# Kernel tuning notes

Hardware: AMD Instinct MI355X
Metric: run time of the kernel (lower is better)

Reference implementation:

```python
import jax, jax.numpy as jnp
import numpy as np

B, S, H, NH = 2, 2048, 2048, 16
HD = H // NH


def setup_inputs() -> dict:
    key = jax.random.key(0)
    ks = jax.random.split(key, 10)
    s = 1.0 / np.sqrt(H)
    x = jax.random.normal(ks[0], (B, S, H), dtype=jnp.float32)
    # additive causal mask: 0 on/below diagonal, -1e9 above
    causal = jnp.tril(jnp.ones((S, S), dtype=bool))
    mask = jnp.where(causal, 0.0, -1e9).astype(jnp.float32)[None, None]
    return {
        "x": x,
        "mask": mask,
        "wq": jax.random.normal(ks[1], (H, H), jnp.float32) * s,
        "bq": jnp.zeros((H,), jnp.float32),
        "wk": jax.random.normal(ks[2], (H, H), jnp.float32) * s,
        "bk": jnp.zeros((H,), jnp.float32),
        "wv": jax.random.normal(ks[3], (H, H), jnp.float32) * s,
        "bv": jnp.zeros((H,), jnp.float32),
        "wo": jax.random.normal(ks[4], (H, H), jnp.float32) * s,
        "bo": jnp.zeros((H,), jnp.float32),
    }


def reference(x, mask, wq, bq, wk, bk, wv, bv, wo, bo):
    b, s, _ = x.shape
    scale = HD ** (-0.5)
    # projections -> [b, nh, s, hd]
    def split_heads(t):
        return t.reshape(b, s, NH, HD).transpose(0, 2, 1, 3)
    q = split_heads(x @ wq + bq)
    k = split_heads(x @ wk + bk)
    v = split_heads(x @ wv + bv)
    scores = jnp.einsum('bhqd,bhkd->bhqk', q, k) * scale + mask
    attn = jax.nn.softmax(scores, axis=-1)
    out = jnp.einsum('bhqk,bhkd->bhqd', attn, v)
    out = out.transpose(0, 2, 1, 3).reshape(b, s, H)
    return out @ wo + bo
```

## Files before the change

### kernel.cpp

```cpp
#include <hip/hip_runtime.h>


using bf16x8 = __attribute__((ext_vector_type(8))) short;
using bf16x4 = __attribute__((ext_vector_type(4))) short;
using f32x4  = __attribute__((ext_vector_type(4))) float;

#define S_LEN 2048
#define NHEAD 16
#define HDIM  128
#define HID   2048

__device__ __forceinline__ unsigned short f2bf(float f) {
    unsigned int u = __float_as_uint(f);
    u += 0x7fffu + ((u >> 16) & 1u);
    return (unsigned short)(u >> 16);
}
__device__ __forceinline__ void gl2lds16(const void* g, void* l) {
    __builtin_amdgcn_global_load_lds(
        (const __attribute__((address_space(1))) void*)g,
        (__attribute__((address_space(3))) void*)l, 16, 0, 0);
}

__device__ __forceinline__ f32x4 pv_mfma(bf16x4 a, bf16x4 b, f32x4 c) {
#if defined(__HIP_DEVICE_COMPILE__)
#if __has_builtin(__builtin_amdgcn_mfma_f32_16x16x16bf16_1k)
    return __builtin_amdgcn_mfma_f32_16x16x16bf16_1k(a, b, c, 0, 0, 0);
#else
    asm("v_mfma_f32_16x16x16_bf16 %0, %1, %2, %0" : "+v"(c) : "v"(a), "v"(b));
    return c;
#endif
#else
    (void)a; (void)b;
    return c;
#endif
}

__global__ void convert_x(const float* __restrict__ x, unsigned short* __restrict__ xb) {
    int i = (blockIdx.x * 256 + threadIdx.x) * 4;
    float4 v = *(const float4*)(x + i);
    ushort4 o;
    o.x = f2bf(v.x); o.y = f2bf(v.y); o.z = f2bf(v.z); o.w = f2bf(v.w);
    *(ushort4*)(xb + i) = o;
}

__global__ void convert_wt(const float* __restrict__ w0, const float* __restrict__ w1,
                           const float* __restrict__ w2, const float* __restrict__ w3,
                           unsigned short* __restrict__ t0, unsigned short* __restrict__ t1,
                           unsigned short* __restrict__ t2, unsigned short* __restrict__ t3) {
    __shared__ float tile[64][65];
    int z = blockIdx.z;
    const float* src = (z == 0) ? w0 : (z == 1) ? w1 : (z == 2) ? w2 : w3;
    unsigned short* dst = (z == 0) ? t0 : (z == 1) ? t1 : (z == 2) ? t2 : t3;
    int r0 = blockIdx.y * 64, c0 = blockIdx.x * 64;
    int t = threadIdx.x;
    for (int i = t; i < 64 * 64; i += 256) {
        int r = i >> 6, c = i & 63;
        tile[r][c] = src[(size_t)(r0 + r) * HID + c0 + c];
    }
    __syncthreads();
    for (int i = t; i < 64 * 64; i += 256) {
        int r = i & 63, c = i >> 6;
        dst[(size_t)(c0 + c) * HID + r0 + r] = f2bf(tile[r][c]);
    }
}

__device__ __forceinline__ void ldfrag(bf16x8* av, bf16x8* bv,
                                       const unsigned short* AD, const unsigned short* BD,
                                       int arow, int brow, int sw) {
    av[0] = *(const bf16x8*)(AD + arow + sw);
    av[1] = *(const bf16x8*)(AD + arow + 1024 + sw);
    av[2] = *(const bf16x8*)(AD + arow + 2048 + sw);
    av[3] = *(const bf16x8*)(AD + arow + 3072 + sw);
    bv[0] = *(const bf16x8*)(BD + brow + sw);
    bv[1] = *(const bf16x8*)(BD + brow + 1024 + sw);
    bv[2] = *(const bf16x8*)(BD + brow + 2048 + sw);
    bv[3] = *(const bf16x8*)(BD + brow + 3072 + sw);
}

__device__ __forceinline__ void mfma16(const bf16x8* av, const bf16x8* bv, f32x4 (&acc)[4][4]) {
#pragma unroll
    for (int mi = 0; mi < 4; ++mi)
#pragma unroll
        for (int jj = 0; jj < 4; ++jj)
            acc[mi][jj] = __builtin_amdgcn_mfma_f32_16x16x32_bf16(av[mi], bv[jj], acc[mi][jj], 0, 0, 0);
}

template <int MODE>
__launch_bounds__(512, 2)
__global__ void gemm8(const unsigned short* __restrict__ A,
                      const unsigned short* __restrict__ Bt0,
                      const unsigned short* __restrict__ Bt1,
                      const unsigned short* __restrict__ Bt2,
                      const float* __restrict__ bias0,
                      const float* __restrict__ bias1,
                      const float* __restrict__ bias2,
                      unsigned short* __restrict__ C0,
                      unsigned short* __restrict__ C1,
                      unsigned short* __restrict__ C2,
                      float* __restrict__ Cf) {
    __shared__ __align__(16) unsigned short lds[49152];
    unsigned short* const A0 = lds;
    unsigned short* const A1 = lds + 8192;
    unsigned short* const B0 = lds + 16384;
    unsigned short* const B1 = lds + 32768;

    const int CPX = (MODE == 1) ? 96 : 32;
    int vb = (blockIdx.x & 7) * CPX + (blockIdx.x >> 3);
    int m0  = (vb & 31) * 128;
    int n0g = (vb >> 5) * 256;

    const unsigned short* Bt = Bt0;
    const float* bias = bias0;
    unsigned short* C = C0;
    int z = 0;
    if (MODE == 1) {
        z = n0g >> 11;
        if (z == 1) { Bt = Bt1; bias = bias1; C = C1; }
        else if (z == 2) { Bt = Bt2; bias = bias2; C = C2; }
    }
    int nb0 = n0g & 2047;

    int tid = threadIdx.x;
    int lane = tid & 63;
    int wv_ = tid >> 6;
    int wr = wv_ >> 2, wc = wv_ & 3;
    int l15 = lane & 15, quad = lane >> 4;

    int tr = tid >> 3;
    int tc = ((tid & 7) ^ (tr & 7)) << 3;
    const unsigned short* gA = A  + (size_t)(m0  + tr) * HID + tc;
    const unsigned short* gB = Bt + (size_t)(nb0 + tr) * HID + tc;
    const int td8 = tid * 8;

    int arow = (wr * 64 + l15) * 64;
    int brow = (wc * 64 + l15) * 64;
    int sw0 = ((quad ^ (l15 & 7)) << 3);
    int sw1 = (((4 + quad) ^ (l15 & 7)) << 3);

    f32x4 acc[4][4];
#pragma unroll
    for (int i = 0; i < 4; ++i)
#pragma unroll
        for (int j = 0; j < 4; ++j) acc[i][j] = (f32x4){0.f, 0.f, 0.f, 0.f};

    bf16x8 avA[4], bvA[4], avB[4], bvB[4];

#define STAGE8(kt, AD, BD) do { int _kc = (kt) * 64;                        \
    gl2lds16(gA + _kc,              (AD) + td8);                            \
    gl2lds16(gA + 64 * HID + _kc,   (AD) + 4096 + td8);                     \
    gl2lds16(gB + _kc,              (BD) + td8);                            \
    gl2lds16(gB + 64 * HID + _kc,   (BD) + 4096 + td8);                     \
    gl2lds16(gB + 128 * HID + _kc,  (BD) + 8192 + td8);                     \
    gl2lds16(gB + 192 * HID + _kc,  (BD) + 12288 + td8); } while (0)

#define SCHED0() __builtin_amdgcn_sched_barrier(0)
#define BAR()   do { asm volatile("" ::: "memory");                                \
                     __builtin_amdgcn_s_barrier();                                 \
                     asm volatile("" ::: "memory"); } while (0)
#define W_LGKM8() do { asm volatile("s_waitcnt lgkmcnt(8)" ::: "memory"); SCHED0(); } while (0)
#define W_LGKM0() do { asm volatile("s_waitcnt lgkmcnt(0)" ::: "memory"); SCHED0(); } while (0)
#define W_VM6()   do { asm volatile("s_waitcnt vmcnt(6)" ::: "memory");   SCHED0(); } while (0)

#define ITER(AD, BD, AN, BN_, ks) do {                                             \
    ldfrag(avB, bvB, AD, BD, arow, brow, sw1);      \
    W_LGKM8();                                                \
    __builtin_amdgcn_s_setprio(1);                                                 \
    mfma16(avA, bvA, acc);                                 \
    __builtin_amdgcn_s_setprio(0);                                                 \
    W_LGKM0();                                      \
    BAR();                                                                         \
    STAGE8(ks, AD, BD);                                \
    W_VM6();                                               \
    BAR();                                                                         \
    ldfrag(avA, bvA, AN, BN_, arow, brow, sw0);   \
    SCHED0();                                                                      \
    __builtin_amdgcn_s_setprio(1);                                                 \
    mfma16(avB, bvB, acc);                            \
    __builtin_amdgcn_s_setprio(0);                                                 \
} while (0)

    STAGE8(0, A0, B0);
    STAGE8(1, A1, B1);
    W_VM6();
    BAR();
    ldfrag(avA, bvA, A0, B0, arow, brow, sw0);

    for (int t = 0; t < 30; t += 2) {
        ITER(A0, B0, A1, B1, t + 2);
        ITER(A1, B1, A0, B0, t + 3);
    }
    ITER(A0, B0, A1, B1, 31);
    ldfrag(avB, bvB, A1, B1, arow, brow, sw1);
    W_LGKM8();
    __builtin_amdgcn_s_setprio(1);
    mfma16(avA, bvA, acc);
    __builtin_amdgcn_s_setprio(0);
    W_LGKM0();
    mfma16(avB, bvB, acc);
    asm volatile("s_waitcnt vmcnt(0)" ::: "memory");

#undef ITER
#undef STAGE8
#undef SCHED0
#undef BAR
#undef W_LGKM8
#undef W_LGKM0
#undef W_VM6

#pragma unroll
    for (int j = 0; j < 4; ++j) {
        int n = nb0 + wc * 64 + j * 16 + l15;
        float bn = bias[n];
#pragma unroll
        for (int i = 0; i < 4; ++i) {
            int mb = m0 + wr * 64 + i * 16 + quad * 4;
            if (MODE == 1 && z == 2) {
                int b = mb >> 11, s = mb & 2047, h = n >> 7, d = n & 127;
                int kt = s >> 4, qv = (s >> 2) & 3, ct = d >> 4, lv = d & 15;
                size_t addr = ((((size_t)((b << 4) + h) * 128 + kt) * 4 + (ct >> 1)) * 4 + qv) * 128
                              + lv * 8 + (ct & 1) * 4;
                ushort4 o;
                o.x = f2bf(acc[i][j][0] + bn);
                o.y = f2bf(acc[i][j][1] + bn);
                o.z = f2bf(acc[i][j][2] + bn);
                o.w = f2bf(acc[i][j][3] + bn);
                *(ushort4*)&C[addr] = o;
            } else {
#pragma unroll
                for (int reg = 0; reg < 4; ++reg) {
                    int m = mb + reg;
                    float v = acc[i][j][reg] + bn;
                    if (MODE == 0) {
                        Cf[(size_t)m * HID + n] = v;
                    } else {
                        int b = m >> 11, s = m & 2047, h = n >> 7, d = n & 127;
                        if (z == 1) {
                            int kt = s >> 4, lk = s & 15, kk = d >> 5, qk = (d >> 3) & 3, e = d & 7;
                            size_t addr = ((((size_t)((b << 4) + h) * 128 + kt) * 4 + kk) * 4 + qk) * 128
                                          + lk * 8 + e;
                            C[addr] = f2bf(v);
                        } else {
                            C[(size_t)(((b << 4) + h) * S_LEN + s) * HDIM + d] = f2bf(v);
                        }
                    }
                }
            }
        }
    }
}

__launch_bounds__(256, 4)
__global__ void attn_kernel(const unsigned short* __restrict__ Qg,
                            const unsigned short* __restrict__ Kp,
                            const unsigned short* __restrict__ Vp,
                            unsigned short* __restrict__ O) {
    int linear = blockIdx.y * 32 + blockIdx.x;
    int xcd = linear & 7;
    int u = linear >> 3;
    int bh = xcd * 4 + (u & 3);
    int j = u >> 2;
    int b = bh >> 4, h = bh & 15;

    int tid = threadIdx.x, lane = tid & 63, w = tid >> 6;
    int l15 = lane & 15, quad = lane >> 4;

    int role = (w + (u >> 5)) & 3;
    int strip = (role < 2) ? (2 * j + role) : (126 - 2 * j + (role - 2));
    int r0 = strip * 16;

    const unsigned short* Qb = Qg + (size_t)bh * (S_LEN * HDIM);
    const unsigned short* Kb = Kp + (size_t)bh * 262144 + quad * 128 + l15 * 8;
    const unsigned short* Vb = Vp + (size_t)bh * 262144 + quad * 128 + l15 * 8;

    bf16x8 qf[4];
#pragma unroll
    for (int kk = 0; kk < 4; ++kk)
        qf[kk] = *(const bf16x8*)&Qb[(size_t)(r0 + l15) * HDIM + kk * 32 + quad * 8];

    f32x4 o_acc[8];
#pragma unroll
    for (int c = 0; c < 8; ++c) o_acc[c] = (f32x4){0.f, 0.f, 0.f, 0.f};
    float l_part = 0.f;

    const float k2 = 0.08838834764831845f * 1.4426950408889634f;

    int nkt = strip + 1;

    bf16x8 kA[4], kB[4], v[4];

#define LOADK(dst, t) do { size_t _o = (size_t)(t) * 2048;                         \
    dst[0] = *(const bf16x8*)&Kb[_o];                                              \
    dst[1] = *(const bf16x8*)&Kb[_o + 512];                                        \
    dst[2] = *(const bf16x8*)&Kb[_o + 1024];                                       \
    dst[3] = *(const bf16x8*)&Kb[_o + 1536]; } while (0)

#define LOADV(dst, t) do { size_t _o = (size_t)(t) * 2048;                         \
    dst[0] = *(const bf16x8*)&Vb[_o];                                              \
    dst[1] = *(const bf16x8*)&Vb[_o + 512];                                        \
    dst[2] = *(const bf16x8*)&Vb[_o + 1024];                                       \
    dst[3] = *(const bf16x8*)&Vb[_o + 1536]; } while (0)

#define VLO(x) __builtin_shufflevector(x, x, 0, 1, 2, 3)
#define VHI(x) __builtin_shufflevector(x, x, 4, 5, 6, 7)

#define TILE(kreg, t) do {                                                         \
    f32x4 st0 = (f32x4){0.f, 0.f, 0.f, 0.f};                                       \
    f32x4 st1 = (f32x4){0.f, 0.f, 0.f, 0.f};                                       \
    st0 = __builtin_amdgcn_mfma_f32_16x16x32_bf16(kreg[0], qf[0], st0, 0, 0, 0);   \
    st1 = __builtin_amdgcn_mfma_f32_16x16x32_bf16(kreg[1], qf[1], st1, 0, 0, 0);   \
    st0 = __builtin_amdgcn_mfma_f32_16x16x32_bf16(kreg[2], qf[2], st0, 0, 0, 0);   \
    st1 = __builtin_amdgcn_mfma_f32_16x16x32_bf16(kreg[3], qf[3], st1, 0, 0, 0);   \
    f32x4 stv = st0 + st1;                                                         \
    float p0, p1, p2, p3;                                                          \
    if ((t) == nkt - 1) {                                                          \
        p0 = (quad * 4 + 0 <= l15) ? exp2f(stv[0] * k2) : 0.f;                     \
        p1 = (quad * 4 + 1 <= l15) ? exp2f(stv[1] * k2) : 0.f;                     \
        p2 = (quad * 4 + 2 <= l15) ? exp2f(stv[2] * k2) : 0.f;                     \
        p3 = (quad * 4 + 3 <= l15) ? exp2f(stv[3] * k2) : 0.f;                     \
    } else {                                                                       \
        p0 = exp2f(stv[0] * k2); p1 = exp2f(stv[1] * k2);                          \
        p2 = exp2f(stv[2] * k2); p3 = exp2f(stv[3] * k2);                          \
    }                                                                              \
    l_part += (p0 + p1) + (p2 + p3);                                               \
    bf16x4 pf;                                                                     \
    pf[0] = (short)f2bf(p0); pf[1] = (short)f2bf(p1);                              \
    pf[2] = (short)f2bf(p2); pf[3] = (short)f2bf(p3);                              \
    o_acc[0] = pv_mfma(pf, VLO(v[0]), o_acc[0]);                                   \
    o_acc[1] = pv_mfma(pf, VHI(v[0]), o_acc[1]);                                   \
    o_acc[2] = pv_mfma(pf, VLO(v[1]), o_acc[2]);                                   \
    o_acc[3] = pv_mfma(pf, VHI(v[1]), o_acc[3]);                                   \
    o_acc[4] = pv_mfma(pf, VLO(v[2]), o_acc[4]);                                   \
    o_acc[5] = pv_mfma(pf, VHI(v[2]), o_acc[5]);                                   \
    o_acc[6] = pv_mfma(pf, VLO(v[3]), o_acc[6]);                                   \
    o_acc[7] = pv_mfma(pf, VHI(v[3]), o_acc[7]);                                   \
} while (0)

    LOADK(kA, 0);
    int kt = 0;
    while (true) {
        int ktn = (kt + 1 < nkt) ? kt + 1 : kt;
        LOADV(v, kt);
        LOADK(kB, ktn);
        TILE(kA, kt);
        if (++kt >= nkt) break;

        ktn = (kt + 1 < nkt) ? kt + 1 : kt;
        LOADV(v, kt);
        LOADK(kA, ktn);
        TILE(kB, kt);
        if (++kt >= nkt) break;
    }

#undef TILE
#undef LOADK
#undef LOADV
#undef VLO
#undef VHI

    l_part += __shfl_xor(l_part, 16, 64);
    l_part += __shfl_xor(l_part, 32, 64);

#pragma unroll
    for (int reg = 0; reg < 4; ++reg) {
        float l = __shfl(l_part, quad * 4 + reg, 64);
        float inv = 1.f / l;
        int srow = r0 + quad * 4 + reg;
        unsigned short* op = O + (size_t)(b * S_LEN + srow) * HID + h * HDIM;
#pragma unroll
        for (int ct = 0; ct < 8; ++ct)
            op[ct * 16 + l15] = f2bf(o_acc[ct][reg] * inv);
    }
}

extern "C" void kernel_launch(void* const* d_in, const int* in_sizes, int n_in,
                              void* d_out, int out_size, void* d_ws, size_t ws_size,
                              hipStream_t stream) {
    (void)in_sizes; (void)n_in; (void)out_size; (void)ws_size;
    const float* x  = (const float*)d_in[0];
    const float* wq = (const float*)d_in[2];
    const float* bq = (const float*)d_in[3];
    const float* wk = (const float*)d_in[4];
    const float* bk = (const float*)d_in[5];
    const float* wv = (const float*)d_in[6];
    const float* bv = (const float*)d_in[7];
    const float* wo = (const float*)d_in[8];
    const float* bo = (const float*)d_in[9];
    float* out = (float*)d_out;

    unsigned short* ws = (unsigned short*)d_ws;
    const size_t WSZ = 4194304;
    unsigned short* wqT = ws;
    unsigned short* wkT = ws + WSZ;
    unsigned short* wvT = ws + 2 * WSZ;
    unsigned short* woT = ws + 3 * WSZ;
    unsigned short* xb  = ws + 4 * WSZ;
    unsigned short* Ab  = ws + 4 * WSZ;
    unsigned short* Qb  = ws + 6 * WSZ;
    unsigned short* Kb  = ws + 8 * WSZ;
    unsigned short* Vb  = ws + 10 * WSZ;

    convert_x<<<dim3(8192), 256, 0, stream>>>(x, xb);
    convert_wt<<<dim3(32, 32, 4), 256, 0, stream>>>(wq, wk, wv, wo, wqT, wkT, wvT, woT);
    gemm8<1><<<dim3(768), 512, 0, stream>>>(xb, wqT, wkT, wvT, bq, bk, bv,
                                            Qb, Kb, Vb, nullptr);
    attn_kernel<<<dim3(32, 32), 256, 0, stream>>>(Qb, Kb, Vb, Ab);
    gemm8<0><<<dim3(256), 512, 0, stream>>>(Ab, woT, nullptr, nullptr,
                                            bo, nullptr, nullptr,
                                            nullptr, nullptr, nullptr, out);
}
```

Measured before the change: 412.0 us.

## Pre-pack weights into MFMA fragment layout and load B directly from global

The weight conversion kernel now writes the bf16 weights in a packed layout that matches the MFMA B-fragment order. The GEMM then loads B fragments straight from global memory into registers instead of staging them through LDS, so only the A tile stays double-buffered in shared memory. The aim is to cut LDS traffic and footprint, which could also raise occupancy. The cost is that B reads now depend on global or L2 latency inside the main loop, and the waitcnt schedule had to be reworked, including a clamped redundant stage at the end of the loop.

```diff
diff --git a/kernel.cpp b/kernel.cpp
--- a/kernel.cpp
+++ b/kernel.cpp
@@ -51,30 +51,28 @@
     int z = blockIdx.z;
     const float* src = (z == 0) ? w0 : (z == 1) ? w1 : (z == 2) ? w2 : w3;
     unsigned short* dst = (z == 0) ? t0 : (z == 1) ? t1 : (z == 2) ? t2 : t3;
-    int r0 = blockIdx.y * 64, c0 = blockIdx.x * 64;
+    int k0 = blockIdx.y * 64, n0 = blockIdx.x * 64;
     int t = threadIdx.x;
     for (int i = t; i < 64 * 64; i += 256) {
         int r = i >> 6, c = i & 63;
-        tile[r][c] = src[(size_t)(r0 + r) * HID + c0 + c];
+        tile[r][c] = src[(size_t)(k0 + r) * HID + n0 + c];
     }
     __syncthreads();
-    for (int i = t; i < 64 * 64; i += 256) {
-        int r = i & 63, c = i >> 6;
-        dst[(size_t)(c0 + c) * HID + r0 + r] = f2bf(tile[r][c]);
-    }
-}
-
-__device__ __forceinline__ void ldfrag(bf16x8* av, bf16x8* bv,
-                                       const unsigned short* AD, const unsigned short* BD,
-                                       int arow, int brow, int sw) {
-    av[0] = *(const bf16x8*)(AD + arow + sw);
-    av[1] = *(const bf16x8*)(AD + arow + 1024 + sw);
-    av[2] = *(const bf16x8*)(AD + arow + 2048 + sw);
-    av[3] = *(const bf16x8*)(AD + arow + 3072 + sw);
-    bv[0] = *(const bf16x8*)(BD + brow + sw);
-    bv[1] = *(const bf16x8*)(BD + brow + 1024 + sw);
-    bv[2] = *(const bf16x8*)(BD + brow + 2048 + sw);
-    bv[3] = *(const bf16x8*)(BD + brow + 3072 + sw);
+    for (int it = 0; it < 2; ++it) {
+        int job = it * 256 + t;
+        int nl = job & 63, k8 = job >> 6;
+        int n = n0 + nl, k = k0 + k8 * 8;
+        size_t base = ((((size_t)(n >> 4) * 64 + (k >> 5)) * 4 + ((k >> 3) & 3)) * 128)
+                      + (size_t)(n & 15) * 8;
+        int kl = k8 * 8;
+        ushort4 o1, o2;
+        o1.x = f2bf(tile[kl + 0][nl]); o1.y = f2bf(tile[kl + 1][nl]);
+        o1.z = f2bf(tile[kl + 2][nl]); o1.w = f2bf(tile[kl + 3][nl]);
+        o2.x = f2bf(tile[kl + 4][nl]); o2.y = f2bf(tile[kl + 5][nl]);
+        o2.z = f2bf(tile[kl + 6][nl]); o2.w = f2bf(tile[kl + 7][nl]);
+        *(ushort4*)&dst[base]     = o1;
+        *(ushort4*)&dst[base + 4] = o2;
+    }
 }
 
 __device__ __forceinline__ void mfma16(const bf16x8* av, const bf16x8* bv, f32x4 (&acc)[4][4]) {
@@ -88,9 +86,9 @@
 template <int MODE>
 __launch_bounds__(512, 2)
 __global__ void gemm8(const unsigned short* __restrict__ A,
-                      const unsigned short* __restrict__ Bt0,
-                      const unsigned short* __restrict__ Bt1,
-                      const unsigned short* __restrict__ Bt2,
+                      const unsigned short* __restrict__ Bp0,
+                      const unsigned short* __restrict__ Bp1,
+                      const unsigned short* __restrict__ Bp2,
                       const float* __restrict__ bias0,
                       const float* __restrict__ bias1,
                       const float* __restrict__ bias2,
@@ -98,25 +96,22 @@
                       unsigned short* __restrict__ C1,
                       unsigned short* __restrict__ C2,
                       float* __restrict__ Cf) {
-    __shared__ __align__(16) unsigned short lds[49152];
-    unsigned short* const A0 = lds;
-    unsigned short* const A1 = lds + 8192;
-    unsigned short* const B0 = lds + 16384;
-    unsigned short* const B1 = lds + 32768;
+    __shared__ __align__(16) unsigned short As0[8192];
+    __shared__ __align__(16) unsigned short As1[8192];
 
     const int CPX = (MODE == 1) ? 96 : 32;
     int vb = (blockIdx.x & 7) * CPX + (blockIdx.x >> 3);
     int m0  = (vb & 31) * 128;
     int n0g = (vb >> 5) * 256;
 
-    const unsigned short* Bt = Bt0;
+    const unsigned short* Bp = Bp0;
     const float* bias = bias0;
     unsigned short* C = C0;
     int z = 0;
     if (MODE == 1) {
         z = n0g >> 11;
-        if (z == 1) { Bt = Bt1; bias = bias1; C = C1; }
-        else if (z == 2) { Bt = Bt2; bias = bias2; C = C2; }
+        if (z == 1) { Bp = Bp1; bias = bias1; C = C1; }
+        else if (z == 2) { Bp = Bp2; bias = bias2; C = C2; }
     }
     int nb0 = n0g & 2047;
 
@@ -128,83 +123,87 @@
 
     int tr = tid >> 3;
     int tc = ((tid & 7) ^ (tr & 7)) << 3;
-    const unsigned short* gA = A  + (size_t)(m0  + tr) * HID + tc;
-    const unsigned short* gB = Bt + (size_t)(nb0 + tr) * HID + tc;
+    const unsigned short* gA = A + (size_t)(m0 + tr) * HID + tc;
     const int td8 = tid * 8;
 
     int arow = (wr * 64 + l15) * 64;
-    int brow = (wc * 64 + l15) * 64;
     int sw0 = ((quad ^ (l15 & 7)) << 3);
     int sw1 = (((4 + quad) ^ (l15 & 7)) << 3);
 
+    const unsigned short* Bw = Bp + ((size_t)((nb0 >> 4) + wc * 4) * 64) * 512 + lane * 8;
+
     f32x4 acc[4][4];
 #pragma unroll
     for (int i = 0; i < 4; ++i)
 #pragma unroll
         for (int j = 0; j < 4; ++j) acc[i][j] = (f32x4){0.f, 0.f, 0.f, 0.f};
 
-    bf16x8 avA[4], bvA[4], avB[4], bvB[4];
-
-#define STAGE8(kt, AD, BD) do { int _kc = (kt) * 64;                        \
-    gl2lds16(gA + _kc,              (AD) + td8);                            \
-    gl2lds16(gA + 64 * HID + _kc,   (AD) + 4096 + td8);                     \
-    gl2lds16(gB + _kc,              (BD) + td8);                            \
-    gl2lds16(gB + 64 * HID + _kc,   (BD) + 4096 + td8);                     \
-    gl2lds16(gB + 128 * HID + _kc,  (BD) + 8192 + td8);                     \
-    gl2lds16(gB + 192 * HID + _kc,  (BD) + 12288 + td8); } while (0)
+    bf16x8 avA[4], avB[4], bvA[4], bvB[4];
+
+#define STAGE(kt, AD) do { int _kc = (kt) * 64;                              \
+    gl2lds16(gA + _kc,            (AD) + td8);                               \
+    gl2lds16(gA + 64 * HID + _kc, (AD) + 4096 + td8); } while (0)
+
+#define LDA(dst, AD, sw) do {                                                \
+    dst[0] = *(const bf16x8*)((AD) + arow + (sw));                           \
+    dst[1] = *(const bf16x8*)((AD) + arow + 1024 + (sw));                    \
+    dst[2] = *(const bf16x8*)((AD) + arow + 2048 + (sw));                    \
+    dst[3] = *(const bf16x8*)((AD) + arow + 3072 + (sw)); } while (0)
+
+#define LDB(dst, kc) do { size_t _b = (size_t)(kc) * 512;                    \
+    dst[0] = *(const bf16x8*)&Bw[_b];                                        \
+    dst[1] = *(const bf16x8*)&Bw[_b + 32768];                                \
+    dst[2] = *(const bf16x8*)&Bw[_b + 65536];                                \
+    dst[3] = *(const bf16x8*)&Bw[_b + 98304]; } while (0)
 
 #define SCHED0() __builtin_amdgcn_sched_barrier(0)
-#define BAR()   do { asm volatile("" ::: "memory");                                \
-                     __builtin_amdgcn_s_barrier();                                 \
+#define BAR()   do { asm volatile("" ::: "memory");                          \
+                     __builtin_amdgcn_s_barrier();                           \
                      asm volatile("" ::: "memory"); } while (0)
-#define W_LGKM8() do { asm volatile("s_waitcnt lgkmcnt(8)" ::: "memory"); SCHED0(); } while (0)
+#define W_LGKM4() do { asm volatile("s_waitcnt lgkmcnt(4)" ::: "memory"); SCHED0(); } while (0)
 #define W_LGKM0() do { asm volatile("s_waitcnt lgkmcnt(0)" ::: "memory"); SCHED0(); } while (0)
+#define W_VM4()   do { asm volatile("s_waitcnt vmcnt(4)" ::: "memory");   SCHED0(); } while (0)
 #define W_VM6()   do { asm volatile("s_waitcnt vmcnt(6)" ::: "memory");   SCHED0(); } while (0)
 
-#define ITER(AD, BD, AN, BN_, ks) do {                                             \
-    ldfrag(avB, bvB, AD, BD, arow, brow, sw1);      \
-    W_LGKM8();                                                \
-    __builtin_amdgcn_s_setprio(1);                                                 \
-    mfma16(avA, bvA, acc);                                 \
-    __builtin_amdgcn_s_setprio(0);                                                 \
-    W_LGKM0();                                      \
-    BAR();                                                                         \
-    STAGE8(ks, AD, BD);                                \
-    W_VM6();                                               \
-    BAR();                                                                         \
-    ldfrag(avA, bvA, AN, BN_, arow, brow, sw0);   \
-    SCHED0();                                                                      \
-    __builtin_amdgcn_s_setprio(1);                                                 \
-    mfma16(avB, bvB, acc);                            \
-    __builtin_amdgcn_s_setprio(0);                                                 \
-} while (0)
-
-    STAGE8(0, A0, B0);
-    STAGE8(1, A1, B1);
+    STAGE(0, As0);
+    STAGE(1, As1);
+    LDB(bvA, 0);
     W_VM6();
     BAR();
-    ldfrag(avA, bvA, A0, B0, arow, brow, sw0);
-
-    for (int t = 0; t < 30; t += 2) {
-        ITER(A0, B0, A1, B1, t + 2);
-        ITER(A1, B1, A0, B0, t + 3);
-    }
-    ITER(A0, B0, A1, B1, 31);
-    ldfrag(avB, bvB, A1, B1, arow, brow, sw1);
-    W_LGKM8();
-    __builtin_amdgcn_s_setprio(1);
-    mfma16(avA, bvA, acc);
-    __builtin_amdgcn_s_setprio(0);
-    W_LGKM0();
-    mfma16(avB, bvB, acc);
-    asm volatile("s_waitcnt vmcnt(0)" ::: "memory");
-
-#undef ITER
-#undef STAGE8
+    LDA(avA, As0, sw0);
+
+    for (int t = 0; t < 32; ++t) {
+        unsigned short* D  = (t & 1) ? As1 : As0;
+        unsigned short* N_ = (t & 1) ? As0 : As1;
+        LDB(bvB, 2 * t + 1);
+        LDA(avB, D, sw1);
+        W_LGKM4();
+        W_VM4();
+        __builtin_amdgcn_s_setprio(1);
+        mfma16(avA, bvA, acc);
+        __builtin_amdgcn_s_setprio(0);
+        W_LGKM0();
+        BAR();
+        int ks  = (t + 2 < 32) ? t + 2 : 31;
+        int kcn = (t < 31) ? 2 * t + 2 : 63;
+        STAGE(ks, D);
+        LDB(bvA, kcn);
+        LDA(avA, N_, sw0);
+        W_VM6();
+        __builtin_amdgcn_s_setprio(1);
+        mfma16(avB, bvB, acc);
+        __builtin_amdgcn_s_setprio(0);
+    }
+    asm volatile("s_waitcnt vmcnt(0) lgkmcnt(0)" ::: "memory");
+
+#undef STAGE
+#undef LDA
+#undef LDB
 #undef SCHED0
 #undef BAR
-#undef W_LGKM8
+#undef W_LGKM4
 #undef W_LGKM0
+#undef W_VM4
 #undef W_VM6
 
 #pragma unroll
@@ -389,10 +388,10 @@
 
     unsigned short* ws = (unsigned short*)d_ws;
     const size_t WSZ = 4194304;
-    unsigned short* wqT = ws;
-    unsigned short* wkT = ws + WSZ;
-    unsigned short* wvT = ws + 2 * WSZ;
-    unsigned short* woT = ws + 3 * WSZ;
+    unsigned short* wqP = ws;
+    unsigned short* wkP = ws + WSZ;
+    unsigned short* wvP = ws + 2 * WSZ;
+    unsigned short* woP = ws + 3 * WSZ;
     unsigned short* xb  = ws + 4 * WSZ;
     unsigned short* Ab  = ws + 4 * WSZ;
     unsigned short* Qb  = ws + 6 * WSZ;
@@ -400,11 +399,11 @@
     unsigned short* Vb  = ws + 10 * WSZ;
 
     convert_x<<<dim3(8192), 256, 0, stream>>>(x, xb);
-    convert_wt<<<dim3(32, 32, 4), 256, 0, stream>>>(wq, wk, wv, wo, wqT, wkT, wvT, woT);
-    gemm8<1><<<dim3(768), 512, 0, stream>>>(xb, wqT, wkT, wvT, bq, bk, bv,
+    convert_wt<<<dim3(32, 32, 4), 256, 0, stream>>>(wq, wk, wv, wo, wqP, wkP, wvP, woP);
+    gemm8<1><<<dim3(768), 512, 0, stream>>>(xb, wqP, wkP, wvP, bq, bk, bv,
                                             Qb, Kb, Vb, nullptr);
     attn_kernel<<<dim3(32, 32), 256, 0, stream>>>(Qb, Kb, Vb, Ab);
-    gemm8<0><<<dim3(256), 512, 0, stream>>>(Ab, woT, nullptr, nullptr,
+    gemm8<0><<<dim3(256), 512, 0, stream>>>(Ab, woP, nullptr, nullptr,
                                             bo, nullptr, nullptr,
                                             nullptr, nullptr, nullptr, out);
 }
```

Result: slower. 429.7 us (+4.3%).
